# Kernel tuning notes

Hardware: AMD Instinct MI355X
Metric: run time of the kernel (lower is better)

The kernel has to match this reference:

```python
import jax, jax.numpy as jnp
import numpy as np


def _gru_layer(seq, W_ih_l, W_hh_l, b_ih_l, b_hh_l):
    # seq: [B, T, H]; W_*: [3H, H]; b_*: [3H]
    B, T, H = seq.shape
    # Precompute input-side gate projections for all timesteps at once.
    xg = jnp.einsum('bth,gh->btg', seq, W_ih_l) + b_ih_l  # [B, T, 3H]
    xg = jnp.transpose(xg, (1, 0, 2))  # [T, B, 3H] for scan over time

    def step(h, xg_t):
        hg = h @ W_hh_l.T + b_hh_l  # [B, 3H]
        xr, xz, xn = jnp.split(xg_t, 3, axis=-1)
        hr, hz, hn = jnp.split(hg, 3, axis=-1)
        r = jax.nn.sigmoid(xr + hr)
        z = jax.nn.sigmoid(xz + hz)
        n = jnp.tanh(xn + r * hn)
        h_new = (1.0 - z) * n + z * h
        return h_new, h_new

    h0 = jnp.zeros((B, H), dtype=seq.dtype)
    _, hs = jax.lax.scan(step, h0, xg)  # hs: [T, B, H]
    return jnp.transpose(hs, (1, 0, 2))  # [B, T, H]


def setup_inputs() -> dict:
    key = jax.random.key(0)
    ks = jax.random.split(key, 7)
    B, T, H, L = 128, 1024, 256, 2
    s = 1.0 / np.sqrt(H)
    return {
        'x': jax.random.normal(ks[0], (B, T, H), dtype=jnp.float32),
        'W_ih': jax.random.normal(ks[1], (L, 3 * H, H), dtype=jnp.float32) * s,
        'W_hh': jax.random.normal(ks[2], (L, 3 * H, H), dtype=jnp.float32) * s,
        'b_ih': jax.random.normal(ks[3], (L, 3 * H), dtype=jnp.float32) * s,
        'b_hh': jax.random.normal(ks[4], (L, 3 * H), dtype=jnp.float32) * s,
        'W_fc': jax.random.normal(ks[5], (H, H), dtype=jnp.float32) * s,
        'b_fc': jax.random.normal(ks[6], (H,), dtype=jnp.float32) * s,
    }


def reference(x, W_ih, W_hh, b_ih, b_hh, W_fc, b_fc):
    # Multi-layer GRU (PyTorch gate convention), batch_first.
    seq = x
    num_layers = W_ih.shape[0]
    for l in range(num_layers):
        seq = _gru_layer(seq, W_ih[l], W_hh[l], b_ih[l], b_hh[l])
    last = seq[:, -1, :]  # [B, H]
    out = jax.nn.sigmoid(last @ W_fc.T + b_fc)
    return out
```

## Files before the change

kernel.cpp:

```cpp
#include <hip/hip_runtime.h>
#include <hip/hip_cooperative_groups.h>
#include <stdint.h>

namespace cg = cooperative_groups;

#define T_ 1024
#define H_ 256
#define G_ 768

typedef __attribute__((ext_vector_type(8))) short bf16x8;
typedef __attribute__((ext_vector_type(4))) float f32x4;

__device__ __forceinline__ unsigned short f2bf(float f) {
    union { float f; uint32_t u; } v; v.f = f;
    uint32_t u = v.u;
    return (unsigned short)((u + 0x7FFFu + ((u >> 16) & 1u)) >> 16);
}

__device__ __forceinline__ float sigm(float x) {
    return __builtin_amdgcn_rcpf(1.f + __expf(-x));
}
__device__ __forceinline__ float tanh_f(float x) {
    return __builtin_amdgcn_rcpf(1.f + __expf(-2.f * x)) * 2.f - 1.f;
}

__device__ __forceinline__ unsigned long long pk4bf(float a, float b, float c, float d) {
    uint32_t lo, hi;
    asm("v_cvt_pk_bf16_f32 %0, %1, %2" : "=v"(lo) : "v"(a), "v"(b));
    asm("v_cvt_pk_bf16_f32 %0, %1, %2" : "=v"(hi) : "v"(c), "v"(d));
    return ((unsigned long long)hi << 32) | (unsigned long long)lo;
}

__device__ __forceinline__ unsigned long long pk4bf_sw(float a, float b, float c, float d) {
    return (unsigned long long)f2bf(a)
         | ((unsigned long long)f2bf(b) << 16)
         | ((unsigned long long)f2bf(c) << 32)
         | ((unsigned long long)f2bf(d) << 48);
}

__device__ __forceinline__ void unpk4(unsigned long long v, float* o) {
    uint32_t lo = (uint32_t)v, hi = (uint32_t)(v >> 32);
    union { uint32_t u; float f; } a, b, c, d;
    a.u = lo << 16; b.u = lo & 0xffff0000u;
    c.u = hi << 16; d.u = hi & 0xffff0000u;
    o[0] = a.f; o[1] = b.f; o[2] = c.f; o[3] = d.f;
}

__device__ __forceinline__ void gload_lds16(const void* g, void* l) {
    __builtin_amdgcn_global_load_lds((const __attribute__((address_space(1))) void*)g,
                                     (__attribute__((address_space(3))) void*)l,
                                     16, 0, 0);
}

__global__ void pack_weights(const float* __restrict__ W_ih, const float* __restrict__ W_hh,
                             unsigned short* __restrict__ pIH, unsigned short* __restrict__ pHH)
{
    int idx = blockIdx.x * blockDim.x + threadIdx.x;
    if (idx >= 2 * 8 * 6 * 8 * 64 * 8) return;
    int pos = idx;
    int j = pos & 7;  pos >>= 3;
    int l = pos & 63; pos >>= 6;
    int kt = pos & 7; pos >>= 3;
    int mt = pos % 6; pos /= 6;
    int w = pos & 7;  pos >>= 3;
    int layer = pos;
    int gate = (mt >> 1) * 256 + w * 32 + (mt & 1) * 16 + (l & 15);
    int k = kt * 32 + (j & 3) + ((l >> 4) << 2) + ((j >> 2) << 4);
    size_t src = (size_t)layer * G_ * H_ + (size_t)gate * H_ + k;
    pIH[idx] = f2bf(W_ih[src]);
    pHH[idx] = f2bf(W_hh[src]);
}

template<bool SRC_BF16>
__device__ void gemm_persist(char* smem, cg::grid_group grid, int gb,
                             const void* __restrict__ srcp,
                             const unsigned short* __restrict__ wpack,
                             const float* __restrict__ bih, const float* __restrict__ bhh,
                             unsigned long long* __restrict__ xgring, size_t slotU,
                             int off, int nc, int chunk)
{
    unsigned short* Bt = (unsigned short*)smem;
    const int tid = threadIdx.x;
    const int w = tid >> 6, l = tid & 63;
    const int bblk = gb & 7;
    const int tg = gb >> 3;
    const int b = l & 15, g = l >> 4;

    bf16x8 af[6][8];
    {
        const bf16x8* wp = (const bf16x8*)wpack;
        #pragma unroll
        for (int mt = 0; mt < 6; ++mt)
            #pragma unroll
            for (int kt = 0; kt < 8; ++kt)
                af[mt][kt] = wp[((w * 6 + mt) * 8 + kt) * 64 + l];
    }
    float bsum[6][4];
    #pragma unroll
    for (int mt = 0; mt < 6; ++mt)
        #pragma unroll
        for (int q = 0; q < 4; ++q) {
            int gate = (mt >> 1) * 256 + w * 32 + (mt & 1) * 16 + g * 4 + q;
            bsum[mt][q] = (gate < 512) ? (bih[gate] + bhh[gate]) : bih[gate];
        }

    const int nst = nc + 3;
    for (int s = 0; s < nst; ++s) {
        int cc = s - off;
        if (cc >= 0 && cc < nc) {
            unsigned long long* xg = xgring + (size_t)(cc & 1) * slotU;
            const int tbase = cc * chunk + tg * 8;

            if (!SRC_BF16) {
                const float* x = (const float*)srcp;
                const int t_i = w;
                const int sb = (l >> 2) & 15;
                const int f0 = (l & 3) * 64;
                const float* row = x + ((size_t)(bblk * 16 + sb) * T_ + (tbase + t_i)) * H_ + f0;
                unsigned short* bt = Bt + t_i * 4096;
                #pragma unroll
                for (int i = 0; i < 64; i += 4) {
                    f32x4 v = *(const f32x4*)(row + i);
                    int f = f0 + i;
                    bt[(f + 0) * 16 + sb] = f2bf(v[0]);
                    bt[(f + 1) * 16 + sb] = f2bf(v[1]);
                    bt[(f + 2) * 16 + sb] = f2bf(v[2]);
                    bt[(f + 3) * 16 + sb] = f2bf(v[3]);
                }
            } else {
                const unsigned short* hs = (const unsigned short*)srcp;
                #pragma unroll
                for (int t_i = 0; t_i < 8; ++t_i) {
                    const unsigned short* src = hs + ((size_t)bblk * T_ + (tbase + t_i)) * 4096
                                                   + (size_t)(w * 64 + l) * 8;
                    gload_lds16(src, Bt + t_i * 4096 + w * 512);
                }
            }
            __syncthreads();

            #pragma unroll 1
            for (int t_i = 0; t_i < 8; ++t_i) {
                const unsigned short* bt = Bt + t_i * 4096;
                f32x4 acc[6];
                #pragma unroll
                for (int mt = 0; mt < 6; ++mt) acc[mt] = (f32x4){0.f, 0.f, 0.f, 0.f};
                #pragma unroll
                for (int kt = 0; kt < 8; ++kt) {
                    bf16x8 bf;
                    if (SRC_BF16) {
                        bf = *(const bf16x8*)(bt + kt * 512 + l * 8);
                    } else {
                        #pragma unroll
                        for (int j = 0; j < 8; ++j) {
                            int k = kt * 32 + (j & 3) + (g << 2) + ((j >> 2) << 4);
                            bf[j] = (short)bt[k * 16 + b];
                        }
                    }
                    #pragma unroll
                    for (int mt = 0; mt < 6; ++mt)
                        acc[mt] = __builtin_amdgcn_mfma_f32_16x16x32_bf16(af[mt][kt], bf, acc[mt], 0, 0, 0);
                }
                unsigned long long* dst = xg + ((size_t)(tg * 8 + t_i) * 8 + bblk) * 3072 + (size_t)w * 384;
                #pragma unroll
                for (int mt = 0; mt < 6; ++mt)
                    dst[mt * 64 + l] = pk4bf_sw(acc[mt][0] + bsum[mt][0], acc[mt][1] + bsum[mt][1],
                                                acc[mt][2] + bsum[mt][2], acc[mt][3] + bsum[mt][3]);
            }
        }
        grid.sync();
    }
}

__device__ void recur_persist(char* smem, cg::grid_group grid, int layer, int bblk,
                              const unsigned long long* __restrict__ xgring, size_t slotU,
                              const unsigned short* __restrict__ wpack,
                              const float* __restrict__ bhh,
                              unsigned short* __restrict__ hseq, float* __restrict__ h2last,
                              int off, int nc, int chunk)
{
    unsigned short* wlds  = (unsigned short*)smem;
    unsigned short* hfrag = (unsigned short*)(smem + 49152);
    const int tid = threadIdx.x;
    const int w = tid >> 6, l = tid & 63;
    const int g = l >> 4, b = l & 15;

    bf16x8 af[6][7];
    {
        const bf16x8* wp = (const bf16x8*)wpack;
        #pragma unroll
        for (int mt = 0; mt < 6; ++mt)
            #pragma unroll
            for (int kt = 0; kt < 7; ++kt) {
                af[mt][kt] = wp[((w * 6 + mt) * 8 + kt) * 64 + l];
                asm volatile("" : "+v"(af[mt][kt]));
            }
    }
    #pragma unroll
    for (int mt = 0; mt < 6; ++mt)
        gload_lds16(wpack + ((((size_t)(w * 6 + mt)) * 8 + 7) * 64 + l) * 8,
                    wlds + (w * 6 + mt) * 512);

    float nbh[2][4];
    #pragma unroll
    for (int s = 0; s < 2; ++s)
        #pragma unroll
        for (int q = 0; q < 4; ++q)
            nbh[s][q] = bhh[512 + w * 32 + s * 16 + g * 4 + q];

    float hreg[2][4];
    #pragma unroll
    for (int s = 0; s < 2; ++s)
        #pragma unroll
        for (int q = 0; q < 4; ++q) hreg[s][q] = 0.f;
    *(unsigned long long*)(&hfrag[(size_t)w * 512 + l * 8])     = 0ull;
    *(unsigned long long*)(&hfrag[(size_t)w * 512 + l * 8 + 4]) = 0ull;
    __syncthreads();

    const int nst = nc + 3;
    for (int s = 0; s < nst; ++s) {
        int cc = s - off;
        if (cc >= 0 && cc < nc) {
            const unsigned long long* xg = xgring + (size_t)(cc & 1) * slotU;
            const int t0 = cc * chunk;

            unsigned long long xgA[6], xgB[6];
            {
                const unsigned long long* xv = xg + (size_t)bblk * 3072 + (size_t)w * 384;
                #pragma unroll
                for (int mt = 0; mt < 6; ++mt) xgA[mt] = xv[mt * 64 + l];
            }

            auto rstep = [&](int it, unsigned long long (&cur)[6], unsigned long long (&nxt)[6]) {
                const int pr = it & 1;
                const unsigned short* hb = hfrag + (size_t)pr * 4096;
                f32x4 acc[6];
                #pragma unroll
                for (int mt = 0; mt < 6; ++mt) acc[mt] = (f32x4){0.f, 0.f, 0.f, 0.f};
                #pragma unroll
                for (int kp = 0; kp < 3; ++kp) {
                    bf16x8 h0 = *(const bf16x8*)(hb + (2 * kp) * 512 + l * 8);
                    bf16x8 h1 = *(const bf16x8*)(hb + (2 * kp + 1) * 512 + l * 8);
                    #pragma unroll
                    for (int mt = 0; mt < 6; ++mt)
                        acc[mt] = __builtin_amdgcn_mfma_f32_16x16x32_bf16(af[mt][2 * kp], h0, acc[mt], 0, 0, 0);
                    #pragma unroll
                    for (int mt = 0; mt < 6; ++mt)
                        acc[mt] = __builtin_amdgcn_mfma_f32_16x16x32_bf16(af[mt][2 * kp + 1], h1, acc[mt], 0, 0, 0);
                }
                {
                    bf16x8 h0 = *(const bf16x8*)(hb + 6 * 512 + l * 8);
                    bf16x8 h1 = *(const bf16x8*)(hb + 7 * 512 + l * 8);
                    #pragma unroll
                    for (int mt = 0; mt < 6; ++mt)
                        acc[mt] = __builtin_amdgcn_mfma_f32_16x16x32_bf16(af[mt][6], h0, acc[mt], 0, 0, 0);
                    #pragma unroll
                    for (int mt = 0; mt < 6; ++mt) {
                        bf16x8 a = *(const bf16x8*)(wlds + (w * 6 + mt) * 512 + l * 8);
                        acc[mt] = __builtin_amdgcn_mfma_f32_16x16x32_bf16(a, h1, acc[mt], 0, 0, 0);
                    }
                }
                unsigned long long pks[2];
                #pragma unroll
                for (int ss = 0; ss < 2; ++ss) {
                    float cx0[4], cx1[4], cx2[4];
                    unpk4(cur[0 + ss], cx0);
                    unpk4(cur[2 + ss], cx1);
                    unpk4(cur[4 + ss], cx2);
                    float hn4[4];
                    #pragma unroll
                    for (int q = 0; q < 4; ++q) {
                        float r = sigm(cx0[q] + acc[0 + ss][q]);
                        float z = sigm(cx1[q] + acc[2 + ss][q]);
                        float n = tanh_f(cx2[q] + r * (acc[4 + ss][q] + nbh[ss][q]));
                        float hn = n + z * (hreg[ss][q] - n);
                        hreg[ss][q] = hn;
                        hn4[q] = hn;
                    }
                    pks[ss] = pk4bf(hn4[0], hn4[1], hn4[2], hn4[3]);
                }
                *(unsigned long long*)(&hfrag[(size_t)(pr ^ 1) * 4096 + w * 512 + l * 8])     = pks[0];
                *(unsigned long long*)(&hfrag[(size_t)(pr ^ 1) * 4096 + w * 512 + l * 8 + 4]) = pks[1];
                if (layer == 0) {
                    unsigned long long* dv = (unsigned long long*)(hseq
                        + ((size_t)bblk * T_ + (t0 + it)) * 4096 + (size_t)w * 512 + l * 8);
                    dv[0] = pks[0];
                    dv[1] = pks[1];
                }
                {
                    int itn = (it + 1 < chunk) ? (it + 1) : it;
                    const unsigned long long* xv = xg + ((size_t)itn * 8 + bblk) * 3072 + (size_t)w * 384;
                    #pragma unroll
                    for (int mt = 0; mt < 6; ++mt) nxt[mt] = xv[mt * 64 + l];
                }
                asm volatile("s_waitcnt lgkmcnt(0)\n\ts_barrier" ::: "memory");
            };

            #pragma unroll 1
            for (int it2 = 0; it2 < chunk; it2 += 2) {
                rstep(it2,     xgA, xgB);
                rstep(it2 + 1, xgB, xgA);
            }
        }
        grid.sync();
    }

    if (layer == 1) {
        #pragma unroll
        for (int s = 0; s < 2; ++s)
            #pragma unroll
            for (int q = 0; q < 4; ++q) {
                int hid = w * 32 + s * 16 + g * 4 + q;
                h2last[(size_t)(bblk * 16 + b) * H_ + hid] = hreg[s][q];
            }
    }
}

__global__ __launch_bounds__(512, 2)
void pipeline(int nc, int chunk,
              const float* __restrict__ x,
              const unsigned short* __restrict__ pIH0, const unsigned short* __restrict__ pIH1,
              const unsigned short* __restrict__ pHH0, const unsigned short* __restrict__ pHH1,
              const float* __restrict__ bih0, const float* __restrict__ bhh0,
              const float* __restrict__ bih1, const float* __restrict__ bhh1,
              unsigned long long* __restrict__ xg0, unsigned long long* __restrict__ xg1,
              unsigned short* __restrict__ hseq, float* __restrict__ h2last)
{
    extern __shared__ char smem[];
    cg::grid_group grid = cg::this_grid();
    const size_t slotU = (size_t)chunk * 24576;
    const int bid = blockIdx.x;
    if (bid < 8) {
        recur_persist(smem, grid, 0, bid, xg0, slotU, pHH0, bhh0, hseq, nullptr, 1, nc, chunk);
    } else if (bid < 16) {
        recur_persist(smem, grid, 1, bid - 8, xg1, slotU, pHH1, bhh1, nullptr, h2last, 3, nc, chunk);
    } else if (bid < 16 + chunk) {
        gemm_persist<true>(smem, grid, bid - 16, hseq, pIH1, bih1, bhh1, xg1, slotU, 2, nc, chunk);
    } else {
        gemm_persist<false>(smem, grid, bid - 16 - chunk, x, pIH0, bih0, bhh0, xg0, slotU, 0, nc, chunk);
    }
}

__global__ void fc_out(const float* __restrict__ h2, const float* __restrict__ W_fc,
                       const float* __restrict__ b_fc, float* __restrict__ out)
{
    __shared__ float hrow[256];
    const int bb = blockIdx.x, i = threadIdx.x;
    hrow[i] = h2[(size_t)bb * 256 + i];
    __syncthreads();
    float acc = b_fc[i];
    const float* wr = W_fc + (size_t)i * 256;
    #pragma unroll 8
    for (int k = 0; k < 256; ++k) acc += hrow[k] * wr[k];
    out[(size_t)bb * 256 + i] = sigm(acc);
}

extern "C" void kernel_launch(void* const* d_in, const int* in_sizes, int n_in,
                              void* d_out, int out_size, void* d_ws, size_t ws_size,
                              hipStream_t stream)
{
    const float* x    = (const float*)d_in[0];
    const float* W_ih = (const float*)d_in[1];
    const float* W_hh = (const float*)d_in[2];
    const float* b_ih = (const float*)d_in[3];
    const float* b_hh = (const float*)d_in[4];
    const float* W_fc = (const float*)d_in[5];
    const float* b_fc = (const float*)d_in[6];
    float* out = (float*)d_out;

    const size_t HSEQ_B = (size_t)8 * T_ * 4096 * 2;
    const size_t PACK_B = 393216ull * 2;
    const size_t H2_B = 131072;
    size_t fixed = HSEQ_B + 2 * PACK_B + H2_B;
    int chunk = 32;
    while (chunk > 8 && fixed + (size_t)chunk * 196608 * 4 > ws_size) chunk >>= 1;
    const size_t slotB = (size_t)chunk * 196608;

    char* ws = (char*)d_ws;
    unsigned long long* xg0 = (unsigned long long*)ws;
    unsigned long long* xg1 = (unsigned long long*)(ws + 2 * slotB);
    size_t off = 4 * slotB;
    unsigned short* hseq = (unsigned short*)(ws + off); off += HSEQ_B;
    unsigned short* pIH  = (unsigned short*)(ws + off); off += PACK_B;
    unsigned short* pHH  = (unsigned short*)(ws + off); off += PACK_B;
    float* h2      = (float*)(ws + off);

    pack_weights<<<1536, 256, 0, stream>>>(W_ih, W_hh, pIH, pHH);

    const unsigned short* pIH0 = pIH;
    const unsigned short* pIH1 = pIH + 196608;
    const unsigned short* pHH0 = pHH;
    const unsigned short* pHH1 = pHH + 196608;
    const float* bih0 = b_ih;
    const float* bih1 = b_ih + G_;
    const float* bhh0 = b_hh;
    const float* bhh1 = b_hh + G_;

    int nc = T_ / chunk;
    int grid = 16 + 2 * chunk;
    void* args[] = {
        (void*)&nc, (void*)&chunk, (void*)&x,
        (void*)&pIH0, (void*)&pIH1, (void*)&pHH0, (void*)&pHH1,
        (void*)&bih0, (void*)&bhh0, (void*)&bih1, (void*)&bhh1,
        (void*)&xg0, (void*)&xg1, (void*)&hseq, (void*)&h2
    };
    hipLaunchCooperativeKernel((const void*)pipeline, dim3(grid), dim3(512),
                               args, 65536, stream);

    fc_out<<<128, 256, 0, stream>>>(h2, W_fc, b_fc, out);
}
```

Before: 2.093 ms.

## Replace grid-wide barriers with per-chunk dataflow flags between pipeline stages

```diff
diff --git a/kernel.cpp b/kernel.cpp
--- a/kernel.cpp
+++ b/kernel.cpp
@@ -1,8 +1,5 @@
 #include <hip/hip_runtime.h>
-#include <hip/hip_cooperative_groups.h>
 #include <stdint.h>
-
-namespace cg = cooperative_groups;
 
 #define T_ 1024
 #define H_ 256
@@ -50,6 +47,14 @@
     __builtin_amdgcn_global_load_lds((const __attribute__((address_space(1))) void*)g,
                                      (__attribute__((address_space(3))) void*)l,
                                      16, 0, 0);
+}
+
+__device__ __forceinline__ void spin_ge(int* p, int target) {
+    while (__hip_atomic_load(p, __ATOMIC_ACQUIRE, __HIP_MEMORY_SCOPE_AGENT) < target)
+        __builtin_amdgcn_s_sleep(16);
+}
+__device__ __forceinline__ void flag_add(int* p) {
+    __hip_atomic_fetch_add(p, 1, __ATOMIC_RELEASE, __HIP_MEMORY_SCOPE_AGENT);
 }
 
 __global__ void pack_weights(const float* __restrict__ W_ih, const float* __restrict__ W_hh,
@@ -72,12 +77,14 @@
 }
 
 template<bool SRC_BF16>
-__device__ void gemm_persist(char* smem, cg::grid_group grid, int gb,
+__device__ void gemm_persist(char* smem, int gb,
                              const void* __restrict__ srcp,
                              const unsigned short* __restrict__ wpack,
                              const float* __restrict__ bih, const float* __restrict__ bhh,
                              unsigned long long* __restrict__ xgring, size_t slotU,
-                             int off, int nc, int chunk)
+                             int nc, int chunk,
+                             int* srcReady, int srcTarget,
+                             int* ringFree, int ringTarget, int* doneCtr)
 {
     unsigned short* Bt = (unsigned short*)smem;
     const int tid = threadIdx.x;
@@ -104,79 +111,83 @@
             bsum[mt][q] = (gate < 512) ? (bih[gate] + bhh[gate]) : bih[gate];
         }
 
-    const int nst = nc + 3;
-    for (int s = 0; s < nst; ++s) {
-        int cc = s - off;
-        if (cc >= 0 && cc < nc) {
-            unsigned long long* xg = xgring + (size_t)(cc & 1) * slotU;
-            const int tbase = cc * chunk + tg * 8;
-
-            if (!SRC_BF16) {
-                const float* x = (const float*)srcp;
-                const int t_i = w;
-                const int sb = (l >> 2) & 15;
-                const int f0 = (l & 3) * 64;
-                const float* row = x + ((size_t)(bblk * 16 + sb) * T_ + (tbase + t_i)) * H_ + f0;
-                unsigned short* bt = Bt + t_i * 4096;
-                #pragma unroll
-                for (int i = 0; i < 64; i += 4) {
-                    f32x4 v = *(const f32x4*)(row + i);
-                    int f = f0 + i;
-                    bt[(f + 0) * 16 + sb] = f2bf(v[0]);
-                    bt[(f + 1) * 16 + sb] = f2bf(v[1]);
-                    bt[(f + 2) * 16 + sb] = f2bf(v[2]);
-                    bt[(f + 3) * 16 + sb] = f2bf(v[3]);
+    for (int cc = 0; cc < nc; ++cc) {
+        if (tid == 0) {
+            if (srcReady) spin_ge(srcReady + cc * 16, srcTarget);
+            if (cc >= 2) spin_ge(ringFree + (cc - 2) * 16, ringTarget);
+        }
+        __syncthreads();
+
+        unsigned long long* xg = xgring + (size_t)(cc & 1) * slotU;
+        const int tbase = cc * chunk + tg * 8;
+
+        if (!SRC_BF16) {
+            const float* x = (const float*)srcp;
+            const int t_i = w;
+            const int sb = (l >> 2) & 15;
+            const int f0 = (l & 3) * 64;
+            const float* row = x + ((size_t)(bblk * 16 + sb) * T_ + (tbase + t_i)) * H_ + f0;
+            unsigned short* bt = Bt + t_i * 4096;
+            #pragma unroll
+            for (int i = 0; i < 64; i += 4) {
+                f32x4 v = *(const f32x4*)(row + i);
+                int f = f0 + i;
+                bt[(f + 0) * 16 + sb] = f2bf(v[0]);
+                bt[(f + 1) * 16 + sb] = f2bf(v[1]);
+                bt[(f + 2) * 16 + sb] = f2bf(v[2]);
+                bt[(f + 3) * 16 + sb] = f2bf(v[3]);
+            }
+        } else {
+            const unsigned short* hs = (const unsigned short*)srcp;
+            #pragma unroll
+            for (int t_i = 0; t_i < 8; ++t_i) {
+                const unsigned short* src = hs + ((size_t)bblk * T_ + (tbase + t_i)) * 4096
+                                               + (size_t)(w * 64 + l) * 8;
+                gload_lds16(src, Bt + t_i * 4096 + w * 512);
+            }
+        }
+        __syncthreads();
+
+        #pragma unroll 1
+        for (int t_i = 0; t_i < 8; ++t_i) {
+            const unsigned short* bt = Bt + t_i * 4096;
+            f32x4 acc[6];
+            #pragma unroll
+            for (int mt = 0; mt < 6; ++mt) acc[mt] = (f32x4){0.f, 0.f, 0.f, 0.f};
+            #pragma unroll
+            for (int kt = 0; kt < 8; ++kt) {
+                bf16x8 bf;
+                if (SRC_BF16) {
+                    bf = *(const bf16x8*)(bt + kt * 512 + l * 8);
+                } else {
+                    #pragma unroll
+                    for (int j = 0; j < 8; ++j) {
+                        int k = kt * 32 + (j & 3) + (g << 2) + ((j >> 2) << 4);
+                        bf[j] = (short)bt[k * 16 + b];
+                    }
                 }
-            } else {
-                const unsigned short* hs = (const unsigned short*)srcp;
-                #pragma unroll
-                for (int t_i = 0; t_i < 8; ++t_i) {
-                    const unsigned short* src = hs + ((size_t)bblk * T_ + (tbase + t_i)) * 4096
-                                                   + (size_t)(w * 64 + l) * 8;
-                    gload_lds16(src, Bt + t_i * 4096 + w * 512);
-                }
-            }
-            __syncthreads();
-
-            #pragma unroll 1
-            for (int t_i = 0; t_i < 8; ++t_i) {
-                const unsigned short* bt = Bt + t_i * 4096;
-                f32x4 acc[6];
-                #pragma unroll
-                for (int mt = 0; mt < 6; ++mt) acc[mt] = (f32x4){0.f, 0.f, 0.f, 0.f};
-                #pragma unroll
-                for (int kt = 0; kt < 8; ++kt) {
-                    bf16x8 bf;
-                    if (SRC_BF16) {
-                        bf = *(const bf16x8*)(bt + kt * 512 + l * 8);
-                    } else {
-                        #pragma unroll
-                        for (int j = 0; j < 8; ++j) {
-                            int k = kt * 32 + (j & 3) + (g << 2) + ((j >> 2) << 4);
-                            bf[j] = (short)bt[k * 16 + b];
-                        }
-                    }
-                    #pragma unroll
-                    for (int mt = 0; mt < 6; ++mt)
-                        acc[mt] = __builtin_amdgcn_mfma_f32_16x16x32_bf16(af[mt][kt], bf, acc[mt], 0, 0, 0);
-                }
-                unsigned long long* dst = xg + ((size_t)(tg * 8 + t_i) * 8 + bblk) * 3072 + (size_t)w * 384;
                 #pragma unroll
                 for (int mt = 0; mt < 6; ++mt)
-                    dst[mt * 64 + l] = pk4bf_sw(acc[mt][0] + bsum[mt][0], acc[mt][1] + bsum[mt][1],
-                                                acc[mt][2] + bsum[mt][2], acc[mt][3] + bsum[mt][3]);
-            }
-        }
-        grid.sync();
-    }
-}
-
-__device__ void recur_persist(char* smem, cg::grid_group grid, int layer, int bblk,
+                    acc[mt] = __builtin_amdgcn_mfma_f32_16x16x32_bf16(af[mt][kt], bf, acc[mt], 0, 0, 0);
+            }
+            unsigned long long* dst = xg + ((size_t)(tg * 8 + t_i) * 8 + bblk) * 3072 + (size_t)w * 384;
+            #pragma unroll
+            for (int mt = 0; mt < 6; ++mt)
+                dst[mt * 64 + l] = pk4bf_sw(acc[mt][0] + bsum[mt][0], acc[mt][1] + bsum[mt][1],
+                                            acc[mt][2] + bsum[mt][2], acc[mt][3] + bsum[mt][3]);
+        }
+        __syncthreads();
+        if (tid == 0) flag_add(doneCtr + cc * 16);
+    }
+}
+
+__device__ void recur_persist(char* smem, int layer, int bblk,
                               const unsigned long long* __restrict__ xgring, size_t slotU,
                               const unsigned short* __restrict__ wpack,
                               const float* __restrict__ bhh,
                               unsigned short* __restrict__ hseq, float* __restrict__ h2last,
-                              int off, int nc, int chunk)
+                              int nc, int chunk,
+                              int* srcReady, int srcTarget, int* doneCtr)
 {
     unsigned short* wlds  = (unsigned short*)smem;
     unsigned short* hfrag = (unsigned short*)(smem + 49152);
@@ -216,92 +227,93 @@
     *(unsigned long long*)(&hfrag[(size_t)w * 512 + l * 8 + 4]) = 0ull;
     __syncthreads();
 
-    const int nst = nc + 3;
-    for (int s = 0; s < nst; ++s) {
-        int cc = s - off;
-        if (cc >= 0 && cc < nc) {
-            const unsigned long long* xg = xgring + (size_t)(cc & 1) * slotU;
-            const int t0 = cc * chunk;
-
-            unsigned long long xgA[6], xgB[6];
+    for (int cc = 0; cc < nc; ++cc) {
+        if (tid == 0) spin_ge(srcReady + cc * 16, srcTarget);
+        __syncthreads();
+
+        const unsigned long long* xg = xgring + (size_t)(cc & 1) * slotU;
+        const int t0 = cc * chunk;
+
+        unsigned long long xgA[6], xgB[6];
+        {
+            const unsigned long long* xv = xg + (size_t)bblk * 3072 + (size_t)w * 384;
+            #pragma unroll
+            for (int mt = 0; mt < 6; ++mt) xgA[mt] = xv[mt * 64 + l];
+        }
+
+        auto rstep = [&](int it, unsigned long long (&cur)[6], unsigned long long (&nxt)[6]) {
+            const int pr = it & 1;
+            const unsigned short* hb = hfrag + (size_t)pr * 4096;
+            f32x4 acc[6];
+            #pragma unroll
+            for (int mt = 0; mt < 6; ++mt) acc[mt] = (f32x4){0.f, 0.f, 0.f, 0.f};
+            #pragma unroll
+            for (int kp = 0; kp < 3; ++kp) {
+                bf16x8 h0 = *(const bf16x8*)(hb + (2 * kp) * 512 + l * 8);
+                bf16x8 h1 = *(const bf16x8*)(hb + (2 * kp + 1) * 512 + l * 8);
+                #pragma unroll
+                for (int mt = 0; mt < 6; ++mt)
+                    acc[mt] = __builtin_amdgcn_mfma_f32_16x16x32_bf16(af[mt][2 * kp], h0, acc[mt], 0, 0, 0);
+                #pragma unroll
+                for (int mt = 0; mt < 6; ++mt)
+                    acc[mt] = __builtin_amdgcn_mfma_f32_16x16x32_bf16(af[mt][2 * kp + 1], h1, acc[mt], 0, 0, 0);
+            }
             {
-                const unsigned long long* xv = xg + (size_t)bblk * 3072 + (size_t)w * 384;
-                #pragma unroll
-                for (int mt = 0; mt < 6; ++mt) xgA[mt] = xv[mt * 64 + l];
-            }
-
-            auto rstep = [&](int it, unsigned long long (&cur)[6], unsigned long long (&nxt)[6]) {
-                const int pr = it & 1;
-                const unsigned short* hb = hfrag + (size_t)pr * 4096;
-                f32x4 acc[6];
-                #pragma unroll
-                for (int mt = 0; mt < 6; ++mt) acc[mt] = (f32x4){0.f, 0.f, 0.f, 0.f};
-                #pragma unroll
-                for (int kp = 0; kp < 3; ++kp) {
-                    bf16x8 h0 = *(const bf16x8*)(hb + (2 * kp) * 512 + l * 8);
-                    bf16x8 h1 = *(const bf16x8*)(hb + (2 * kp + 1) * 512 + l * 8);
-                    #pragma unroll
-                    for (int mt = 0; mt < 6; ++mt)
-                        acc[mt] = __builtin_amdgcn_mfma_f32_16x16x32_bf16(af[mt][2 * kp], h0, acc[mt], 0, 0, 0);
-                    #pragma unroll
-                    for (int mt = 0; mt < 6; ++mt)
-                        acc[mt] = __builtin_amdgcn_mfma_f32_16x16x32_bf16(af[mt][2 * kp + 1], h1, acc[mt], 0, 0, 0);
+                bf16x8 h0 = *(const bf16x8*)(hb + 6 * 512 + l * 8);
+                bf16x8 h1 = *(const bf16x8*)(hb + 7 * 512 + l * 8);
+                #pragma unroll
+                for (int mt = 0; mt < 6; ++mt)
+                    acc[mt] = __builtin_amdgcn_mfma_f32_16x16x32_bf16(af[mt][6], h0, acc[mt], 0, 0, 0);
+                #pragma unroll
+                for (int mt = 0; mt < 6; ++mt) {
+                    bf16x8 a = *(const bf16x8*)(wlds + (w * 6 + mt) * 512 + l * 8);
+                    acc[mt] = __builtin_amdgcn_mfma_f32_16x16x32_bf16(a, h1, acc[mt], 0, 0, 0);
                 }
-                {
-                    bf16x8 h0 = *(const bf16x8*)(hb + 6 * 512 + l * 8);
-                    bf16x8 h1 = *(const bf16x8*)(hb + 7 * 512 + l * 8);
-                    #pragma unroll
-                    for (int mt = 0; mt < 6; ++mt)
-                        acc[mt] = __builtin_amdgcn_mfma_f32_16x16x32_bf16(af[mt][6], h0, acc[mt], 0, 0, 0);
-                    #pragma unroll
-                    for (int mt = 0; mt < 6; ++mt) {
-                        bf16x8 a = *(const bf16x8*)(wlds + (w * 6 + mt) * 512 + l * 8);
-                        acc[mt] = __builtin_amdgcn_mfma_f32_16x16x32_bf16(a, h1, acc[mt], 0, 0, 0);
-                    }
+            }
+            unsigned long long pks[2];
+            #pragma unroll
+            for (int ss = 0; ss < 2; ++ss) {
+                float cx0[4], cx1[4], cx2[4];
+                unpk4(cur[0 + ss], cx0);
+                unpk4(cur[2 + ss], cx1);
+                unpk4(cur[4 + ss], cx2);
+                float hn4[4];
+                #pragma unroll
+                for (int q = 0; q < 4; ++q) {
+                    float r = sigm(cx0[q] + acc[0 + ss][q]);
+                    float z = sigm(cx1[q] + acc[2 + ss][q]);
+                    float n = tanh_f(cx2[q] + r * (acc[4 + ss][q] + nbh[ss][q]));
+                    float hn = n + z * (hreg[ss][q] - n);
+                    hreg[ss][q] = hn;
+                    hn4[q] = hn;
                 }
-                unsigned long long pks[2];
-                #pragma unroll
-                for (int ss = 0; ss < 2; ++ss) {
-                    float cx0[4], cx1[4], cx2[4];
-                    unpk4(cur[0 + ss], cx0);
-                    unpk4(cur[2 + ss], cx1);
-                    unpk4(cur[4 + ss], cx2);
-                    float hn4[4];
-                    #pragma unroll
-                    for (int q = 0; q < 4; ++q) {
-                        float r = sigm(cx0[q] + acc[0 + ss][q]);
-                        float z = sigm(cx1[q] + acc[2 + ss][q]);
-                        float n = tanh_f(cx2[q] + r * (acc[4 + ss][q] + nbh[ss][q]));
-                        float hn = n + z * (hreg[ss][q] - n);
-                        hreg[ss][q] = hn;
-                        hn4[q] = hn;
-                    }
-                    pks[ss] = pk4bf(hn4[0], hn4[1], hn4[2], hn4[3]);
-                }
-                *(unsigned long long*)(&hfrag[(size_t)(pr ^ 1) * 4096 + w * 512 + l * 8])     = pks[0];
-                *(unsigned long long*)(&hfrag[(size_t)(pr ^ 1) * 4096 + w * 512 + l * 8 + 4]) = pks[1];
-                if (layer == 0) {
-                    unsigned long long* dv = (unsigned long long*)(hseq
-                        + ((size_t)bblk * T_ + (t0 + it)) * 4096 + (size_t)w * 512 + l * 8);
-                    dv[0] = pks[0];
-                    dv[1] = pks[1];
-                }
-                {
-                    int itn = (it + 1 < chunk) ? (it + 1) : it;
-                    const unsigned long long* xv = xg + ((size_t)itn * 8 + bblk) * 3072 + (size_t)w * 384;
-                    #pragma unroll
-                    for (int mt = 0; mt < 6; ++mt) nxt[mt] = xv[mt * 64 + l];
-                }
-                asm volatile("s_waitcnt lgkmcnt(0)\n\ts_barrier" ::: "memory");
-            };
-
-            #pragma unroll 1
-            for (int it2 = 0; it2 < chunk; it2 += 2) {
-                rstep(it2,     xgA, xgB);
-                rstep(it2 + 1, xgB, xgA);
-            }
-        }
-        grid.sync();
+                pks[ss] = pk4bf(hn4[0], hn4[1], hn4[2], hn4[3]);
+            }
+            *(unsigned long long*)(&hfrag[(size_t)(pr ^ 1) * 4096 + w * 512 + l * 8])     = pks[0];
+            *(unsigned long long*)(&hfrag[(size_t)(pr ^ 1) * 4096 + w * 512 + l * 8 + 4]) = pks[1];
+            if (layer == 0) {
+                unsigned long long* dv = (unsigned long long*)(hseq
+                    + ((size_t)bblk * T_ + (t0 + it)) * 4096 + (size_t)w * 512 + l * 8);
+                dv[0] = pks[0];
+                dv[1] = pks[1];
+            }
+            {
+                int itn = (it + 1 < chunk) ? (it + 1) : it;
+                const unsigned long long* xv = xg + ((size_t)itn * 8 + bblk) * 3072 + (size_t)w * 384;
+                #pragma unroll
+                for (int mt = 0; mt < 6; ++mt) nxt[mt] = xv[mt * 64 + l];
+            }
+            asm volatile("s_waitcnt lgkmcnt(0)\n\ts_barrier" ::: "memory");
+        };
+
+        #pragma unroll 1
+        for (int it2 = 0; it2 < chunk; it2 += 2) {
+            rstep(it2,     xgA, xgB);
+            rstep(it2 + 1, xgB, xgA);
+        }
+
+        __syncthreads();
+        if (tid == 0) flag_add(doneCtr + cc * 16);
     }
 
     if (layer == 1) {
@@ -323,20 +335,28 @@
               const float* __restrict__ bih0, const float* __restrict__ bhh0,
               const float* __restrict__ bih1, const float* __restrict__ bhh1,
               unsigned long long* __restrict__ xg0, unsigned long long* __restrict__ xg1,
-              unsigned short* __restrict__ hseq, float* __restrict__ h2last)
+              unsigned short* __restrict__ hseq, float* __restrict__ h2last,
+              int* __restrict__ flags)
 {
     extern __shared__ char smem[];
-    cg::grid_group grid = cg::this_grid();
     const size_t slotU = (size_t)chunk * 24576;
+    int* g0done = flags;
+    int* rdone0 = flags + 2048;
+    int* g1done = flags + 4096;
+    int* rdone1 = flags + 6144;
     const int bid = blockIdx.x;
     if (bid < 8) {
-        recur_persist(smem, grid, 0, bid, xg0, slotU, pHH0, bhh0, hseq, nullptr, 1, nc, chunk);
+        recur_persist(smem, 0, bid, xg0, slotU, pHH0, bhh0, hseq, nullptr,
+                      nc, chunk, g0done, chunk, rdone0);
     } else if (bid < 16) {
-        recur_persist(smem, grid, 1, bid - 8, xg1, slotU, pHH1, bhh1, nullptr, h2last, 3, nc, chunk);
+        recur_persist(smem, 1, bid - 8, xg1, slotU, pHH1, bhh1, nullptr, h2last,
+                      nc, chunk, g1done, chunk, rdone1);
     } else if (bid < 16 + chunk) {
-        gemm_persist<true>(smem, grid, bid - 16, hseq, pIH1, bih1, bhh1, xg1, slotU, 2, nc, chunk);
+        gemm_persist<true>(smem, bid - 16, hseq, pIH1, bih1, bhh1, xg1, slotU,
+                           nc, chunk, rdone0, 8, rdone1, 8, g1done);
     } else {
-        gemm_persist<false>(smem, grid, bid - 16 - chunk, x, pIH0, bih0, bhh0, xg0, slotU, 0, nc, chunk);
+        gemm_persist<false>(smem, bid - 16 - chunk, x, pIH0, bih0, bhh0, xg0, slotU,
+                            nc, chunk, nullptr, 0, rdone0, 8, g0done);
     }
 }
 
@@ -370,7 +390,8 @@
     const size_t HSEQ_B = (size_t)8 * T_ * 4096 * 2;
     const size_t PACK_B = 393216ull * 2;
     const size_t H2_B = 131072;
-    size_t fixed = HSEQ_B + 2 * PACK_B + H2_B;
+    const size_t FLG_B = 32768;
+    size_t fixed = HSEQ_B + 2 * PACK_B + H2_B + FLG_B;
     int chunk = 32;
     while (chunk > 8 && fixed + (size_t)chunk * 196608 * 4 > ws_size) chunk >>= 1;
     const size_t slotB = (size_t)chunk * 196608;
@@ -382,8 +403,10 @@
     unsigned short* hseq = (unsigned short*)(ws + off); off += HSEQ_B;
     unsigned short* pIH  = (unsigned short*)(ws + off); off += PACK_B;
     unsigned short* pHH  = (unsigned short*)(ws + off); off += PACK_B;
-    float* h2      = (float*)(ws + off);
-
+    float* h2     = (float*)(ws + off); off += H2_B;
+    int* flags    = (int*)(ws + off);
+
+    hipMemsetAsync(flags, 0, FLG_B, stream);
     pack_weights<<<1536, 256, 0, stream>>>(W_ih, W_hh, pIH, pHH);
 
     const unsigned short* pIH0 = pIH;
@@ -401,7 +424,7 @@
         (void*)&nc, (void*)&chunk, (void*)&x,
         (void*)&pIH0, (void*)&pIH1, (void*)&pHH0, (void*)&pHH1,
         (void*)&bih0, (void*)&bhh0, (void*)&bih1, (void*)&bhh1,
-        (void*)&xg0, (void*)&xg1, (void*)&hseq, (void*)&h2
+        (void*)&xg0, (void*)&xg1, (void*)&hseq, (void*)&h2, (void*)&flags
     };
     hipLaunchCooperativeKernel((const void*)pipeline, dim3(grid), dim3(512),
                                args, 65536, stream);
```

New measurement: 1.943 ms. 1.08x faster.
